# Kernel optimization log

Measured on AMD Instinct MI355X. Metric: run time of the kernel, lower is better.

Reference implementation:

```python
import jax, jax.numpy as jnp
import numpy as np

EPS = 1e-6


def _row_normalize(x):
    return x / (jnp.linalg.norm(x, axis=1, keepdims=True) + EPS)


def _cluster(data, mu, cluster_temp, num_iter):
    # data: [N, D], mu: [K, D]
    data = _row_normalize(data)
    dist = data @ mu.T  # placeholder; overwritten in loop (num_iter >= 1 always here)
    for _ in range(num_iter):
        mu = _row_normalize(mu)
        dist = data @ mu.T                      # [N, K] skinny matmul
        r = jax.nn.softmax(cluster_temp * dist, axis=1)
        cluster_r = r.sum(axis=0)               # [K]
        cluster_mean = r.T @ data               # [K, D]
        mu = cluster_mean / cluster_r[:, None]  # == diag(1/cluster_r) @ cluster_mean
    r = jax.nn.softmax(cluster_temp * dist, axis=1)
    return mu, r


def setup_inputs() -> dict:
    key = jax.random.key(0)
    k1, k2 = jax.random.split(key)
    N, D, K = 200000, 128, 64
    embeds = jax.random.normal(k1, (N, D), dtype=jnp.float32)
    init = jax.random.uniform(k2, (K, D), dtype=jnp.float32)  # torch.rand(K, nout)
    return {"embeds": embeds, "init": init, "cluster_temp": 30}


def reference(embeds, init, cluster_temp):
    temp = jnp.asarray(cluster_temp, dtype=embeds.dtype)
    mu_init, _ = _cluster(embeds, init, temp, num_iter=10)
    mu, r = _cluster(embeds, jax.lax.stop_gradient(mu_init), temp, num_iter=1)
    return mu, r
```

## Files before the change

kernel.cpp:

```cpp
#include <hip/hip_runtime.h>

#define D 128
#define K 64
#define NROWS 200000
#define RT_ROWS 64
#define NTILES (NROWS / RT_ROWS)
#define TPB 256
#define NBLK 512
#define TILE_BYTES 49152
#define PSLOT2 8320
#define NIT 11

typedef __attribute__((ext_vector_type(8))) short bf16x8;
typedef __attribute__((ext_vector_type(4))) float f32x4;

#define XH  0
#define XL  16384
#define XTO 32768
#define RTT 49152
#define RSO 57344
#define LDS_BYTES 58368

__device__ __forceinline__ int xrow_off(int row, int dim) {
  return (row * 256 + dim * 2) ^ ((row & 7) << 4);
}
__device__ __forceinline__ int xt_off(int dim, int row) {
  return (dim * 128 + row * 2) ^ ((dim & 7) << 4);
}
__device__ __forceinline__ int rt_off(int c, int row) {
  return (c * 128 + row * 2) ^ ((c & 7) << 4);
}
__device__ __forceinline__ ushort f2bf(float x) {
  uint u = __float_as_uint(x);
  return (ushort)((u + 0x7FFF + ((u >> 16) & 1)) >> 16);
}
__device__ __forceinline__ float bf2f(ushort b) {
  return __uint_as_float(((uint)b) << 16);
}
__device__ __forceinline__ float dot4(const float4 a, const float4 b) {
  return a.x * b.x + a.y * b.y + a.z * b.z + a.w * b.w;
}
__device__ __forceinline__ void gload16(const char* g, char* l) {
  __builtin_amdgcn_global_load_lds(
      (__attribute__((address_space(1))) void*)(g),
      (__attribute__((address_space(3))) void*)(l), 16, 0, 0);
}

__global__ __launch_bounds__(TPB) void prep_kernel(
    const float* __restrict__ data, char* __restrict__ prep)
{
  __shared__ __align__(16) char smem[TILE_BYTES];
  const int t = threadIdx.x;
  const int tile = blockIdx.x;
  const int row = t >> 2, d0 = (t & 3) * 32;

  const float4* src = (const float4*)(data + (size_t)(tile * RT_ROWS + row) * D + d0);
  float xf[32];
  float ss = 0.f;
#pragma unroll
  for (int i = 0; i < 8; ++i) {
    float4 v = src[i];
    ss += dot4(v, v);
    xf[4 * i] = v.x; xf[4 * i + 1] = v.y; xf[4 * i + 2] = v.z; xf[4 * i + 3] = v.w;
  }
  ss += __shfl_xor(ss, 1);
  ss += __shfl_xor(ss, 2);
  const float inv = 1.f / (sqrtf(ss) + 1e-6f);

  ushort hs[32], ls[32];
#pragma unroll
  for (int e = 0; e < 32; ++e) {
    const float a = xf[e] * inv;
    const ushort h = f2bf(a);
    hs[e] = h;
    ls[e] = f2bf(a - bf2f(h));
  }
#pragma unroll
  for (int j = 0; j < 4; ++j) {
    uint hp[4], lp[4];
#pragma unroll
    for (int q = 0; q < 4; ++q) {
      hp[q] = (uint)hs[8*j + 2*q] | ((uint)hs[8*j + 2*q + 1] << 16);
      lp[q] = (uint)ls[8*j + 2*q] | ((uint)ls[8*j + 2*q + 1] << 16);
    }
    *(uint4*)(smem + XH + xrow_off(row, d0 + 8*j)) = make_uint4(hp[0], hp[1], hp[2], hp[3]);
    *(uint4*)(smem + XL + xrow_off(row, d0 + 8*j)) = make_uint4(lp[0], lp[1], lp[2], lp[3]);
  }
#pragma unroll
  for (int e = 0; e < 32; ++e)
    *(ushort*)(smem + XTO + xt_off(d0 + e, row)) = hs[e];
  __syncthreads();
  char* gout = prep + (size_t)tile * TILE_BYTES;
#pragma unroll
  for (int i = 0; i < 12; ++i)
    *(uint4*)(gout + i * 4096 + t * 16) = *(const uint4*)(smem + i * 4096 + t * 16);
}

__global__ __launch_bounds__(TPB, 2) void pass_kernel(
    const char* __restrict__ prep, const float* __restrict__ mu_src,
    const int* __restrict__ temp_p, float* __restrict__ acc_slot,
    float* __restrict__ r_out, const int write_r)
{
  __shared__ __align__(16) char smem[LDS_BYTES];
  const int t = threadIdx.x;
  const int w = t >> 6, l = t & 63, lg = l >> 4, lr = l & 15;
  const float temp = (float)(*temp_p);

  {
    const int row = t >> 2, d0 = (t & 3) * 32;
    const float4* src = (const float4*)(mu_src + row * D + d0);
    float mf[32];
    float ss = 0.f;
#pragma unroll
    for (int i = 0; i < 8; ++i) {
      float4 v = src[i];
      ss += dot4(v, v);
      mf[4*i] = v.x; mf[4*i+1] = v.y; mf[4*i+2] = v.z; mf[4*i+3] = v.w;
    }
    ss += __shfl_xor(ss, 1);
    ss += __shfl_xor(ss, 2);
    const float inv = 1.f / (sqrtf(ss) + 1e-6f);
#pragma unroll
    for (int j = 0; j < 4; ++j) {
      uint hp[4], lp[4];
#pragma unroll
      for (int q = 0; q < 4; ++q) {
        const float a0 = mf[8*j + 2*q] * inv, a1 = mf[8*j + 2*q + 1] * inv;
        const ushort h0 = f2bf(a0), h1 = f2bf(a1);
        const ushort g0 = f2bf(a0 - bf2f(h0)), g1 = f2bf(a1 - bf2f(h1));
        hp[q] = (uint)h0 | ((uint)h1 << 16);
        lp[q] = (uint)g0 | ((uint)g1 << 16);
      }
      *(uint4*)(smem + XH + xrow_off(row, d0 + 8*j)) = make_uint4(hp[0], hp[1], hp[2], hp[3]);
      *(uint4*)(smem + XL + xrow_off(row, d0 + 8*j)) = make_uint4(lp[0], lp[1], lp[2], lp[3]);
    }
  }
  __syncthreads();
  bf16x8 muh[4][4], mul[4][4];
#pragma unroll
  for (int kc = 0; kc < 4; ++kc)
#pragma unroll
    for (int ns = 0; ns < 4; ++ns) {
      muh[kc][ns] = *(const bf16x8*)(smem + XH + xrow_off(16*ns + lr, kc*32 + lg*8));
      mul[kc][ns] = *(const bf16x8*)(smem + XL + xrow_off(16*ns + lr, kc*32 + lg*8));
    }
  __syncthreads();

  f32x4 accm[4][2];
#pragma unroll
  for (int ms = 0; ms < 4; ++ms)
#pragma unroll
    for (int n2 = 0; n2 < 2; ++n2) accm[ms][n2] = (f32x4){0.f, 0.f, 0.f, 0.f};
  float rsum[4] = {0.f, 0.f, 0.f, 0.f};

  for (int tile = blockIdx.x; tile < NTILES; tile += NBLK) {
    const char* g = prep + (size_t)tile * TILE_BYTES + w * 1024 + l * 16;
#pragma unroll
    for (int i = 0; i < 12; ++i)
      gload16(g + i * 4096, smem + i * 4096 + w * 1024);
    __syncthreads();

    f32x4 pacc[4];
#pragma unroll
    for (int ns = 0; ns < 4; ++ns) pacc[ns] = (f32x4){0.f, 0.f, 0.f, 0.f};
#pragma unroll
    for (int kc = 0; kc < 4; ++kc) {
      const int doff = kc * 32 + lg * 8;
      const bf16x8 ah = *(const bf16x8*)(smem + XH + xrow_off(16*w + lr, doff));
      const bf16x8 al = *(const bf16x8*)(smem + XL + xrow_off(16*w + lr, doff));
#pragma unroll
      for (int ns = 0; ns < 4; ++ns) {
        pacc[ns] = __builtin_amdgcn_mfma_f32_16x16x32_bf16(ah, muh[kc][ns], pacc[ns], 0, 0, 0);
        pacc[ns] = __builtin_amdgcn_mfma_f32_16x16x32_bf16(al, muh[kc][ns], pacc[ns], 0, 0, 0);
        pacc[ns] = __builtin_amdgcn_mfma_f32_16x16x32_bf16(ah, mul[kc][ns], pacc[ns], 0, 0, 0);
      }
    }

    float rv[4][4], sinv[4];
#pragma unroll
    for (int j = 0; j < 4; ++j) {
      float sj = 0.f;
#pragma unroll
      for (int ns = 0; ns < 4; ++ns) { rv[ns][j] = __expf(temp * pacc[ns][j]); sj += rv[ns][j]; }
      sj += __shfl_xor(sj, 1); sj += __shfl_xor(sj, 2);
      sj += __shfl_xor(sj, 4); sj += __shfl_xor(sj, 8);
      sinv[j] = 1.f / sj;
    }
#pragma unroll
    for (int ns = 0; ns < 4; ++ns) {
      const float r0 = rv[ns][0]*sinv[0], r1 = rv[ns][1]*sinv[1],
                  r2 = rv[ns][2]*sinv[2], r3 = rv[ns][3]*sinv[3];
      const ushort h0 = f2bf(r0), h1 = f2bf(r1), h2 = f2bf(r2), h3 = f2bf(r3);
      rsum[ns] += (bf2f(h0) + bf2f(h1)) + (bf2f(h2) + bf2f(h3));
      *(uint2*)(smem + RTT + rt_off(16*ns + lr, 16*w + lg*4)) =
          make_uint2((uint)h0 | ((uint)h1 << 16), (uint)h2 | ((uint)h3 << 16));
      if (write_r) {
        const size_t rb = (size_t)tile * RT_ROWS + 16*w + lg*4;
        r_out[(rb + 0) * K + 16*ns + lr] = r0;
        r_out[(rb + 1) * K + 16*ns + lr] = r1;
        r_out[(rb + 2) * K + 16*ns + lr] = r2;
        r_out[(rb + 3) * K + 16*ns + lr] = r3;
      }
    }
    __syncthreads();

#pragma unroll
    for (int kc2 = 0; kc2 < 2; ++kc2) {
      const int k0 = kc2 * 32 + lg * 8;
      bf16x8 af[4];
#pragma unroll
      for (int ms = 0; ms < 4; ++ms)
        af[ms] = *(const bf16x8*)(smem + RTT + rt_off(16*ms + lr, k0));
#pragma unroll
      for (int n2 = 0; n2 < 2; ++n2) {
        const int dim = 32*w + 16*n2 + lr;
        const bf16x8 bv = *(const bf16x8*)(smem + XTO + xt_off(dim, k0));
#pragma unroll
        for (int ms = 0; ms < 4; ++ms)
          accm[ms][n2] = __builtin_amdgcn_mfma_f32_16x16x32_bf16(af[ms], bv, accm[ms][n2], 0, 0, 0);
      }
    }
    __syncthreads();
  }

#pragma unroll
  for (int ms = 0; ms < 4; ++ms)
#pragma unroll
    for (int n2 = 0; n2 < 2; ++n2)
#pragma unroll
      for (int j = 0; j < 4; ++j)
        atomicAdd(&acc_slot[(16*ms + lg*4 + j) * D + 32*w + 16*n2 + lr], accm[ms][n2][j]);
#pragma unroll
  for (int ns = 0; ns < 4; ++ns) {
    rsum[ns] += __shfl_xor(rsum[ns], 16);
    rsum[ns] += __shfl_xor(rsum[ns], 32);
  }
  float* rs = (float*)(smem + RSO);
  if (lg == 0)
#pragma unroll
    for (int ns = 0; ns < 4; ++ns) rs[w * K + 16*ns + lr] = rsum[ns];
  __syncthreads();
  if (t < K)
    atomicAdd(&acc_slot[K*D + t], (rs[t] + rs[K + t]) + (rs[2*K + t] + rs[3*K + t]));
}

__global__ __launch_bounds__(TPB) void final_kernel(
    const float* __restrict__ slot, float* __restrict__ mu_out)
{
  const int idx = blockIdx.x * TPB + threadIdx.x;
  mu_out[idx] = slot[idx] / slot[K * D + (idx >> 7)];
}

extern "C" void kernel_launch(void* const* d_in, const int* in_sizes, int n_in,
                              void* d_out, int out_size, void* d_ws, size_t ws_size,
                              hipStream_t stream)
{
  const float* data = (const float*)d_in[0];
  const float* init = (const float*)d_in[1];
  const int* temp_p = (const int*)d_in[2];
  float* out = (float*)d_out;

  char* prep = (char*)d_ws;
  float* slots = (float*)(prep + (size_t)NTILES * TILE_BYTES);

  hipMemsetAsync(slots, 0, (size_t)NIT * PSLOT2 * sizeof(float), stream);
  prep_kernel<<<dim3(NTILES), dim3(TPB), 0, stream>>>(data, prep);

  for (int it = 0; it < NIT; ++it) {
    const float* mu_src = (it == 0) ? init : (slots + (size_t)(it - 1) * PSLOT2);
    pass_kernel<<<dim3(NBLK), dim3(TPB), 0, stream>>>(
        prep, mu_src, temp_p, slots + (size_t)it * PSLOT2, out + K*D, it == NIT - 1);
  }
  final_kernel<<<dim3(32), dim3(TPB), 0, stream>>>(
      slots + (size_t)(NIT - 1) * PSLOT2, out);
}
```

Measured before the change: 702.6 us.

## Double-buffer tile loads, shard atomic accumulators, write prep directly to global

The pass kernel now prefetches the next tile with global-to-LDS loads while computing the current one. The transposed X tile is double-buffered, and explicit waitcnt/barriers replace the full syncthreads pairs. Atomic accumulation is spread over 16 sub-slots to cut contention, and those sub-slots are summed when the next pass loads mu and in the final kernel. The prep kernel writes hi/lo rows straight to global and builds the transpose from LDS. This raises LDS use, which may lower occupancy, and the hand-written vmcnt accounting risks correctness.

```diff
diff --git a/kernel.cpp b/kernel.cpp
--- a/kernel.cpp
+++ b/kernel.cpp
@@ -9,6 +9,8 @@
 #define NBLK 512
 #define TILE_BYTES 49152
 #define PSLOT2 8320
+#define SUB 16
+#define SLOT_STRIDE (SUB * PSLOT2)
 #define NIT 11
 
 typedef __attribute__((ext_vector_type(8))) short bf16x8;
@@ -16,10 +18,11 @@
 
 #define XH  0
 #define XL  16384
-#define XTO 32768
-#define RTT 49152
-#define RSO 57344
-#define LDS_BYTES 58368
+#define XT0 32768
+#define XT1 49152
+#define RTT 65536
+#define RSO 73728
+#define LDS_BYTES 74752
 
 __device__ __forceinline__ int xrow_off(int row, int dim) {
   return (row * 256 + dim * 2) ^ ((row & 7) << 4);
@@ -49,7 +52,7 @@
 __global__ __launch_bounds__(TPB) void prep_kernel(
     const float* __restrict__ data, char* __restrict__ prep)
 {
-  __shared__ __align__(16) char smem[TILE_BYTES];
+  __shared__ __align__(16) char smem[16384];
   const int t = threadIdx.x;
   const int tile = blockIdx.x;
   const int row = t >> 2, d0 = (t & 3) * 32;
@@ -67,39 +70,47 @@
   ss += __shfl_xor(ss, 2);
   const float inv = 1.f / (sqrtf(ss) + 1e-6f);
 
-  ushort hs[32], ls[32];
-#pragma unroll
-  for (int e = 0; e < 32; ++e) {
-    const float a = xf[e] * inv;
-    const ushort h = f2bf(a);
-    hs[e] = h;
-    ls[e] = f2bf(a - bf2f(h));
-  }
+  char* gout = prep + (size_t)tile * TILE_BYTES;
 #pragma unroll
   for (int j = 0; j < 4; ++j) {
     uint hp[4], lp[4];
 #pragma unroll
     for (int q = 0; q < 4; ++q) {
-      hp[q] = (uint)hs[8*j + 2*q] | ((uint)hs[8*j + 2*q + 1] << 16);
-      lp[q] = (uint)ls[8*j + 2*q] | ((uint)ls[8*j + 2*q + 1] << 16);
-    }
-    *(uint4*)(smem + XH + xrow_off(row, d0 + 8*j)) = make_uint4(hp[0], hp[1], hp[2], hp[3]);
-    *(uint4*)(smem + XL + xrow_off(row, d0 + 8*j)) = make_uint4(lp[0], lp[1], lp[2], lp[3]);
-  }
-#pragma unroll
-  for (int e = 0; e < 32; ++e)
-    *(ushort*)(smem + XTO + xt_off(d0 + e, row)) = hs[e];
+      const float a0 = xf[8*j + 2*q] * inv, a1 = xf[8*j + 2*q + 1] * inv;
+      const ushort h0 = f2bf(a0), h1 = f2bf(a1);
+      const ushort g0 = f2bf(a0 - bf2f(h0)), g1 = f2bf(a1 - bf2f(h1));
+      hp[q] = (uint)h0 | ((uint)h1 << 16);
+      lp[q] = (uint)g0 | ((uint)g1 << 16);
+    }
+    const uint4 h4 = make_uint4(hp[0], hp[1], hp[2], hp[3]);
+    const int off = xrow_off(row, d0 + 8*j);
+    *(uint4*)(gout + off) = h4;
+    *(uint4*)(gout + 16384 + off) = make_uint4(lp[0], lp[1], lp[2], lp[3]);
+    *(uint4*)(smem + off) = h4;
+  }
   __syncthreads();
-  char* gout = prep + (size_t)tile * TILE_BYTES;
-#pragma unroll
-  for (int i = 0; i < 12; ++i)
-    *(uint4*)(gout + i * 4096 + t * 16) = *(const uint4*)(smem + i * 4096 + t * 16);
+
+  {
+    const int dim = t & 127, r0 = (t >> 7) * 32;
+#pragma unroll
+    for (int jj = 0; jj < 4; ++jj) {
+      uint p[4];
+#pragma unroll
+      for (int q = 0; q < 4; ++q) {
+        const ushort v0 = *(const ushort*)(smem + xrow_off(r0 + 8*jj + 2*q, dim));
+        const ushort v1 = *(const ushort*)(smem + xrow_off(r0 + 8*jj + 2*q + 1, dim));
+        p[q] = (uint)v0 | ((uint)v1 << 16);
+      }
+      *(uint4*)(gout + 32768 + xt_off(dim, r0 + 8*jj)) =
+          make_uint4(p[0], p[1], p[2], p[3]);
+    }
+  }
 }
 
 __global__ __launch_bounds__(TPB, 2) void pass_kernel(
     const char* __restrict__ prep, const float* __restrict__ mu_src,
-    const int* __restrict__ temp_p, float* __restrict__ acc_slot,
-    float* __restrict__ r_out, const int write_r)
+    const int first, const int* __restrict__ temp_p,
+    float* __restrict__ acc_slot, float* __restrict__ r_out, const int write_r)
 {
   __shared__ __align__(16) char smem[LDS_BYTES];
   const int t = threadIdx.x;
@@ -108,15 +119,29 @@
 
   {
     const int row = t >> 2, d0 = (t & 3) * 32;
-    const float4* src = (const float4*)(mu_src + row * D + d0);
     float mf[32];
+    if (first) {
+      const float4* src = (const float4*)(mu_src + row * D + d0);
+#pragma unroll
+      for (int i = 0; i < 8; ++i) {
+        float4 v = src[i];
+        mf[4*i] = v.x; mf[4*i+1] = v.y; mf[4*i+2] = v.z; mf[4*i+3] = v.w;
+      }
+    } else {
+#pragma unroll
+      for (int e = 0; e < 32; ++e) mf[e] = 0.f;
+      for (int s = 0; s < SUB; ++s) {
+        const float4* p = (const float4*)(mu_src + s * PSLOT2 + row * D + d0);
+#pragma unroll
+        for (int i = 0; i < 8; ++i) {
+          float4 v = p[i];
+          mf[4*i] += v.x; mf[4*i+1] += v.y; mf[4*i+2] += v.z; mf[4*i+3] += v.w;
+        }
+      }
+    }
     float ss = 0.f;
 #pragma unroll
-    for (int i = 0; i < 8; ++i) {
-      float4 v = src[i];
-      ss += dot4(v, v);
-      mf[4*i] = v.x; mf[4*i+1] = v.y; mf[4*i+2] = v.z; mf[4*i+3] = v.w;
-    }
+    for (int e = 0; e < 32; ++e) ss += mf[e] * mf[e];
     ss += __shfl_xor(ss, 1);
     ss += __shfl_xor(ss, 2);
     const float inv = 1.f / (sqrtf(ss) + 1e-6f);
@@ -131,8 +156,9 @@
         hp[q] = (uint)h0 | ((uint)h1 << 16);
         lp[q] = (uint)g0 | ((uint)g1 << 16);
       }
-      *(uint4*)(smem + XH + xrow_off(row, d0 + 8*j)) = make_uint4(hp[0], hp[1], hp[2], hp[3]);
-      *(uint4*)(smem + XL + xrow_off(row, d0 + 8*j)) = make_uint4(lp[0], lp[1], lp[2], lp[3]);
+      const int off = xrow_off(row, d0 + 8*j);
+      *(uint4*)(smem + XT0 + off) = make_uint4(hp[0], hp[1], hp[2], hp[3]);
+      *(uint4*)(smem + XT1 + off) = make_uint4(lp[0], lp[1], lp[2], lp[3]);
     }
   }
   __syncthreads();
@@ -141,8 +167,8 @@
   for (int kc = 0; kc < 4; ++kc)
 #pragma unroll
     for (int ns = 0; ns < 4; ++ns) {
-      muh[kc][ns] = *(const bf16x8*)(smem + XH + xrow_off(16*ns + lr, kc*32 + lg*8));
-      mul[kc][ns] = *(const bf16x8*)(smem + XL + xrow_off(16*ns + lr, kc*32 + lg*8));
+      muh[kc][ns] = *(const bf16x8*)(smem + XT0 + xrow_off(16*ns + lr, kc*32 + lg*8));
+      mul[kc][ns] = *(const bf16x8*)(smem + XT1 + xrow_off(16*ns + lr, kc*32 + lg*8));
     }
   __syncthreads();
 
@@ -153,12 +179,24 @@
     for (int n2 = 0; n2 < 2; ++n2) accm[ms][n2] = (f32x4){0.f, 0.f, 0.f, 0.f};
   float rsum[4] = {0.f, 0.f, 0.f, 0.f};
 
+  asm volatile("s_waitcnt vmcnt(0)" ::: "memory");
+  {
+    const char* g0 = prep + (size_t)blockIdx.x * TILE_BYTES + w * 1024 + l * 16;
+#pragma unroll
+    for (int i = 0; i < 8; ++i) gload16(g0 + i * 4096, smem + XH + i * 4096 + w * 1024);
+#pragma unroll
+    for (int i = 0; i < 4; ++i) gload16(g0 + 32768 + i * 4096, smem + XT0 + i * 4096 + w * 1024);
+  }
+  int cur = 0;
+
   for (int tile = blockIdx.x; tile < NTILES; tile += NBLK) {
-    const char* g = prep + (size_t)tile * TILE_BYTES + w * 1024 + l * 16;
-#pragma unroll
-    for (int i = 0; i < 12; ++i)
-      gload16(g + i * 4096, smem + i * 4096 + w * 1024);
-    __syncthreads();
+    int nxt = tile + NBLK;
+    if (nxt >= NTILES) nxt = tile;
+    const char* gn = prep + (size_t)nxt * TILE_BYTES + w * 1024 + l * 16;
+
+    asm volatile("s_waitcnt vmcnt(4)" ::: "memory");
+    __builtin_amdgcn_sched_barrier(0);
+    __builtin_amdgcn_s_barrier();
 
     f32x4 pacc[4];
 #pragma unroll
@@ -202,34 +240,54 @@
         r_out[(rb + 3) * K + 16*ns + lr] = r3;
       }
     }
-    __syncthreads();
-
-#pragma unroll
-    for (int kc2 = 0; kc2 < 2; ++kc2) {
-      const int k0 = kc2 * 32 + lg * 8;
-      bf16x8 af[4];
-#pragma unroll
-      for (int ms = 0; ms < 4; ++ms)
-        af[ms] = *(const bf16x8*)(smem + RTT + rt_off(16*ms + lr, k0));
-#pragma unroll
-      for (int n2 = 0; n2 < 2; ++n2) {
-        const int dim = 32*w + 16*n2 + lr;
-        const bf16x8 bv = *(const bf16x8*)(smem + XTO + xt_off(dim, k0));
+
+    asm volatile("s_waitcnt lgkmcnt(0)" ::: "memory");
+    __builtin_amdgcn_sched_barrier(0);
+    __builtin_amdgcn_s_barrier();
+
+#pragma unroll
+    for (int i = 0; i < 8; ++i) gload16(gn + i * 4096, smem + XH + i * 4096 + w * 1024);
+
+    asm volatile("s_waitcnt vmcnt(8)" ::: "memory");
+    __builtin_amdgcn_sched_barrier(0);
+    __builtin_amdgcn_s_barrier();
+
+    {
+      char* xtc = smem + (cur ? XT1 : XT0);
+#pragma unroll
+      for (int kc2 = 0; kc2 < 2; ++kc2) {
+        const int k0 = kc2 * 32 + lg * 8;
+        bf16x8 af[4];
 #pragma unroll
         for (int ms = 0; ms < 4; ++ms)
-          accm[ms][n2] = __builtin_amdgcn_mfma_f32_16x16x32_bf16(af[ms], bv, accm[ms][n2], 0, 0, 0);
-      }
-    }
-    __syncthreads();
-  }
-
+          af[ms] = *(const bf16x8*)(smem + RTT + rt_off(16*ms + lr, k0));
+#pragma unroll
+        for (int n2 = 0; n2 < 2; ++n2) {
+          const int dim = 32*w + 16*n2 + lr;
+          const bf16x8 bv = *(const bf16x8*)(xtc + xt_off(dim, k0));
+#pragma unroll
+          for (int ms = 0; ms < 4; ++ms)
+            accm[ms][n2] = __builtin_amdgcn_mfma_f32_16x16x32_bf16(af[ms], bv, accm[ms][n2], 0, 0, 0);
+        }
+      }
+    }
+
+    {
+      char* xtn = smem + (cur ? XT0 : XT1);
+#pragma unroll
+      for (int i = 0; i < 4; ++i) gload16(gn + 32768 + i * 4096, xtn + i * 4096 + w * 1024);
+    }
+    cur ^= 1;
+  }
+
+  float* slot = acc_slot + (size_t)(blockIdx.x & (SUB - 1)) * PSLOT2;
 #pragma unroll
   for (int ms = 0; ms < 4; ++ms)
 #pragma unroll
     for (int n2 = 0; n2 < 2; ++n2)
 #pragma unroll
       for (int j = 0; j < 4; ++j)
-        atomicAdd(&acc_slot[(16*ms + lg*4 + j) * D + 32*w + 16*n2 + lr], accm[ms][n2][j]);
+        atomicAdd(&slot[(16*ms + lg*4 + j) * D + 32*w + 16*n2 + lr], accm[ms][n2][j]);
 #pragma unroll
   for (int ns = 0; ns < 4; ++ns) {
     rsum[ns] += __shfl_xor(rsum[ns], 16);
@@ -241,14 +299,21 @@
     for (int ns = 0; ns < 4; ++ns) rs[w * K + 16*ns + lr] = rsum[ns];
   __syncthreads();
   if (t < K)
-    atomicAdd(&acc_slot[K*D + t], (rs[t] + rs[K + t]) + (rs[2*K + t] + rs[3*K + t]));
+    atomicAdd(&slot[K*D + t], (rs[t] + rs[K + t]) + (rs[2*K + t] + rs[3*K + t]));
 }
 
 __global__ __launch_bounds__(TPB) void final_kernel(
     const float* __restrict__ slot, float* __restrict__ mu_out)
 {
   const int idx = blockIdx.x * TPB + threadIdx.x;
-  mu_out[idx] = slot[idx] / slot[K * D + (idx >> 7)];
+  const int c = idx >> 7;
+  float m = 0.f, r = 0.f;
+#pragma unroll
+  for (int s = 0; s < SUB; ++s) {
+    m += slot[s * PSLOT2 + idx];
+    r += slot[s * PSLOT2 + K * D + c];
+  }
+  mu_out[idx] = m / r;
 }
 
 extern "C" void kernel_launch(void* const* d_in, const int* in_sizes, int n_in,
@@ -263,14 +328,15 @@
   char* prep = (char*)d_ws;
   float* slots = (float*)(prep + (size_t)NTILES * TILE_BYTES);
 
-  hipMemsetAsync(slots, 0, (size_t)NIT * PSLOT2 * sizeof(float), stream);
+  hipMemsetAsync(slots, 0, (size_t)NIT * SLOT_STRIDE * sizeof(float), stream);
   prep_kernel<<<dim3(NTILES), dim3(TPB), 0, stream>>>(data, prep);
 
   for (int it = 0; it < NIT; ++it) {
-    const float* mu_src = (it == 0) ? init : (slots + (size_t)(it - 1) * PSLOT2);
+    const float* mu_src = (it == 0) ? init : (slots + (size_t)(it - 1) * SLOT_STRIDE);
     pass_kernel<<<dim3(NBLK), dim3(TPB), 0, stream>>>(
-        prep, mu_src, temp_p, slots + (size_t)it * PSLOT2, out + K*D, it == NIT - 1);
+        prep, mu_src, (it == 0) ? 1 : 0, temp_p,
+        slots + (size_t)it * SLOT_STRIDE, out + K*D, (it == NIT - 1) ? 1 : 0);
   }
   final_kernel<<<dim3(32), dim3(TPB), 0, stream>>>(
-      slots + (size_t)(NIT - 1) * PSLOT2, out);
-}
+      slots + (size_t)(NIT - 1) * SLOT_STRIDE, out);
+}
```

Result: slower. 820.1 us (+16.7%).
